# Performance work log

Hardware: AMD Instinct MI355X
Metric: run time of the kernel (lower is better)

Reference implementation:

```python
import jax, jax.numpy as jnp
import numpy as np

NUM_CLASSES = 80
AFS = 1024          # actors_features_size
OFS = 2048          # objects_features_size
NHEADS = 4
NHID = AFS // NHEADS + 4 // NHEADS   # 257
D = AFS + 4                           # 1028
ALPHA = 0.2                           # LeakyReLU slope
N_ACT, N_OBJ = 512, 3584


def _gat(x, adj_mask, W, a):
    # x: [N, D]; W: [H, D, NHID]; a: [H, 2*NHID]; adj_mask: [N, N] bool
    Wh = jnp.einsum('nf,hfd->hnd', x, W)                      # [H, N, NHID]
    f1 = jnp.einsum('hnd,hd->hn', Wh, a[:, :NHID])            # src score
    f2 = jnp.einsum('hnd,hd->hn', Wh, a[:, NHID:])            # dst score
    e = f1[:, :, None] + f2[:, None, :]                       # [H, N, N]
    e = jnp.where(e > 0, e, ALPHA * e)                        # LeakyReLU
    e = jnp.where(adj_mask[None], e, jnp.asarray(-9e15, e.dtype))
    att = jax.nn.softmax(e, axis=-1)                          # [H, N, N]
    h = jnp.einsum('hnm,hmd->hnd', att, Wh)                   # [H, N, NHID]
    h = jax.nn.elu(h)
    return jnp.transpose(h, (1, 0, 2)).reshape(x.shape[0], NHEADS * NHID)


def _ln(x, g, b):
    m = jnp.mean(x, axis=-1, keepdims=True)
    v = jnp.mean((x - m) ** 2, axis=-1, keepdims=True)
    return (x - m) * jax.lax.rsqrt(v + 1e-5) * g + b


def setup_inputs() -> dict:
    key = jax.random.key(0)
    ks = jax.random.split(key, 24)
    d = {
        'actors_features': jax.random.normal(ks[0], (N_ACT, 1024, 4, 7, 7), jnp.float32),
        'actors_labels': jax.random.uniform(ks[1], (N_ACT, NUM_CLASSES), jnp.float32),
        'actors_boxes': jax.random.uniform(ks[2], (N_ACT, 4), jnp.float32),
        'objects_features': jax.random.normal(ks[3], (N_OBJ, OFS), jnp.float32),
        'objects_boxes': jax.random.uniform(ks[4], (N_OBJ, 4), jnp.float32),
        'adj': jax.random.randint(ks[5], (N_ACT + N_OBJ, N_ACT + N_OBJ), 0, 2, jnp.int32),
    }
    s = lambda k, shp, fan: jax.random.normal(k, shp, jnp.float32) * (1.0 / np.sqrt(fan))
    d['obj_W'] = s(ks[6], (OFS, AFS), OFS)
    d['obj_b'] = jnp.zeros((AFS,), jnp.float32)
    d['gat1_W'] = s(ks[7], (NHEADS, D, NHID), D)
    d['gat1_a'] = s(ks[8], (NHEADS, 2 * NHID), 2 * NHID)
    d['gat_fc_W'] = s(ks[9], (D, D), D)
    d['gat_fc_b'] = jnp.zeros((D,), jnp.float32)
    d['ln1_g'] = jnp.ones((D,), jnp.float32)
    d['ln1_b'] = jnp.zeros((D,), jnp.float32)
    d['gat2_W'] = s(ks[10], (NHEADS, D, NHID), D)
    d['gat2_a'] = s(ks[11], (NHEADS, 2 * NHID), 2 * NHID)
    d['gat_fc2_W'] = s(ks[12], (D, D), D)
    d['gat_fc2_b'] = jnp.zeros((D,), jnp.float32)
    d['ln2_g'] = jnp.ones((D,), jnp.float32)
    d['ln2_b'] = jnp.zeros((D,), jnp.float32)
    d['logits_W'] = s(ks[13], (D, NUM_CLASSES), D)
    d['logits_b'] = jnp.zeros((NUM_CLASSES,), jnp.float32)
    return d


def reference(actors_features, actors_labels, actors_boxes, objects_features,
              objects_boxes, adj, obj_W, obj_b, gat1_W, gat1_a, gat_fc_W,
              gat_fc_b, ln1_g, ln1_b, gat2_W, gat2_a, gat_fc2_W, gat_fc2_b,
              ln2_g, ln2_b, logits_W, logits_b):
    ab, ob = actors_boxes, objects_boxes
    a_geo = jnp.stack([ab[:, 3] - ab[:, 1], ab[:, 2] - ab[:, 0],
                       (ab[:, 2] - ab[:, 0]) / 2 + ab[:, 0],
                       (ab[:, 3] - ab[:, 1]) / 2 + ab[:, 1]], axis=1)
    o_geo = jnp.stack([ob[:, 3] - ob[:, 1], ob[:, 2] - ob[:, 0],
                       (ob[:, 2] - ob[:, 0]) / 2 + ob[:, 0],
                       (ob[:, 3] - ob[:, 1]) / 2 + ob[:, 1]], axis=1)
    # torch.no_grad mean-pool over T,H,W -> [N, C]
    af = jax.lax.stop_gradient(jnp.mean(actors_features, axis=(2, 3, 4)))
    af = jnp.concatenate([af, a_geo], axis=1)                 # [Na, D]
    of = jax.nn.relu(objects_features @ obj_W + obj_b)        # reducer (OFS>AFS)
    of = jnp.concatenate([of, o_geo], axis=1)                 # [No, D]
    x = jnp.concatenate([af, of], axis=0)                     # [N, D]
    mask = adj > 0
    g = _gat(x, mask, gat1_W, gat1_a)
    x = _ln(x + g @ gat_fc_W + gat_fc_b, ln1_g, ln1_b)
    g = _gat(x, mask, gat2_W, gat2_a)
    x = _ln(x + g @ gat_fc2_W + gat_fc2_b, ln2_g, ln2_b)
    logits = x[:af.shape[0]] @ logits_W + logits_b            # [Na, C]
    y = actors_labels
    loss = jnp.mean(jnp.clip(logits, 0, None) - logits * y
                    + jnp.log1p(jnp.exp(-jnp.abs(logits))))
    return jax.nn.sigmoid(logits), loss
```

## Files before the change

### kernel.cpp

```cpp
#include <hip/hip_runtime.h>
#include <cstdint>

#define NACT 512
#define NOBJ 3584
#define NTOT 4096
#define DCOLS 1028
#define NHID_ 257
#define OFSZ 2048
#define KPAD 1056
#define NPADH 320
#define NPADFC 1088

typedef float f32x4 __attribute__((ext_vector_type(4)));
typedef short short8v __attribute__((ext_vector_type(8)));
typedef short short4v __attribute__((ext_vector_type(4)));

static const size_t OFF_X0    = 0;
static const size_t OFF_T     = 4210688;
static const size_t OFF_F1    = 8421376;
static const size_t OFF_F2    = 8437760;
static const size_t OFF_RMAX  = 8454144;
static const size_t OFF_RDEN  = 8470528;
static const size_t OFF_LOSSP = 8486912;
static const size_t OFF_MASK  = 8487424;
static const size_t OFF_XB    = 9011712;
static const size_t OFF_GB    = 11174400;
static const size_t OFF_OBJWT = 13337088;
static const size_t OFF_GATWT = 14385664;
static const size_t OFF_FCWT  = 15737344;
static const size_t OFF_WHT   = 16886272;

__device__ __forceinline__ short f2bf(float x) {
    unsigned u = __float_as_uint(x);
    u += 0x7fffu + ((u >> 16) & 1u);
    return (short)(u >> 16);
}
__device__ __forceinline__ int swz(int row, int chunk) {
    return row * 64 + (((chunk ^ ((row >> 1) & 3))) << 4);
}

__global__ void k_geo(const float* __restrict__ ab, const float* __restrict__ ob,
                      float* __restrict__ X) {
    int n = blockIdx.x * blockDim.x + threadIdx.x;
    if (n >= NTOT) return;
    const float* b = (n < NACT) ? &ab[n * 4] : &ob[(n - NACT) * 4];
    float x0 = b[0], y0 = b[1], x1 = b[2], y1 = b[3];
    float* o = &X[(size_t)n * DCOLS + 1024];
    o[0] = y1 - y0;
    o[1] = x1 - x0;
    o[2] = (x1 - x0) * 0.5f + x0;
    o[3] = (y1 - y0) * 0.5f + y0;
}

__global__ __launch_bounds__(256) void k_meanpool(const float* __restrict__ af,
                                                  float* __restrict__ X) {
    int w = blockIdx.x * 4 + (threadIdx.x >> 6);
    int lane = threadIdx.x & 63;
    const float* src = af + (size_t)w * 196;
    float s = src[lane] + src[lane + 64] + src[lane + 128];
    if (lane < 4) s += src[192 + lane];
    #pragma unroll
    for (int off = 32; off; off >>= 1) s += __shfl_down(s, off);
    if (lane == 0) {
        int n = w >> 10, c = w & 1023;
        X[(size_t)n * DCOLS + c] = s * (1.0f / 196.0f);
    }
}

__global__ __launch_bounds__(256) void k_packmask(const int* __restrict__ adj,
                                                  unsigned long long* __restrict__ mb) {
    int w = blockIdx.x * 4 + (threadIdx.x >> 6);
    int lane = threadIdx.x & 63;
    int v = adj[(size_t)w * 64 + lane];
    unsigned long long m = __ballot(v > 0);
    if (lane == 0) mb[w] = m;
}

__global__ __launch_bounds__(256) void k_transpW(const float* __restrict__ W, int K, int N,
                                                 short* __restrict__ Wt, int Kpad, int Npad) {
    __shared__ float Ws[32][33];
    int k0 = blockIdx.x * 32, n0 = blockIdx.y * 32;
    int t = threadIdx.x;
    #pragma unroll
    for (int i = 0; i < 4; ++i) {
        int j = t + i * 256;
        int r = j >> 5, c = j & 31;
        float v = 0.f;
        if (k0 + r < K && n0 + c < N) v = W[(size_t)(k0 + r) * N + n0 + c];
        Ws[r][c] = v;
    }
    __syncthreads();
    #pragma unroll
    for (int i = 0; i < 4; ++i) {
        int j = t + i * 256;
        int n = j >> 5, k = j & 31;
        Wt[(size_t)(n0 + n) * Kpad + k0 + k] = f2bf(Ws[k][n]);
    }
}

__global__ __launch_bounds__(256) void k_convX(const float* __restrict__ X,
                                               short* __restrict__ Xb) {
    int i = blockIdx.x * 256 + threadIdx.x;
    int n = i / 132, g = i % 132;
    int c0 = g * 8;
    short8v o;
    if (c0 + 8 <= DCOLS) {
        float4 v0 = *reinterpret_cast<const float4*>(&X[(size_t)n * DCOLS + c0]);
        float4 v1 = *reinterpret_cast<const float4*>(&X[(size_t)n * DCOLS + c0 + 4]);
        o[0]=f2bf(v0.x); o[1]=f2bf(v0.y); o[2]=f2bf(v0.z); o[3]=f2bf(v0.w);
        o[4]=f2bf(v1.x); o[5]=f2bf(v1.y); o[6]=f2bf(v1.z); o[7]=f2bf(v1.w);
    } else {
        #pragma unroll
        for (int j = 0; j < 8; ++j)
            o[j] = (c0 + j < DCOLS) ? f2bf(X[(size_t)n * DCOLS + c0 + j]) : (short)0;
    }
    *reinterpret_cast<short8v*>(&Xb[(size_t)n * KPAD + c0]) = o;
}

template <int MODE>
__global__ __launch_bounds__(256) void k_mm(
    const void* __restrict__ Aptr, int lda,
    const short* __restrict__ Bt, int ldb,
    void* __restrict__ Cptr, int ldc,
    const float* __restrict__ bias,
    const float* __restrict__ resid, int ldr,
    float* __restrict__ F1, float* __restrict__ F2,
    const float* __restrict__ RMAX, const float* __restrict__ RDEN,
    const unsigned long long* __restrict__ MB,
    const float* __restrict__ AV,
    int nk, int Nvalid) {
    __shared__ char sm[12288];
    const int t = threadIdx.x;
    const int m0 = blockIdx.x * 128;
    const int n0 = blockIdx.y * 64;
    const int z = blockIdx.z;

    short* Cwh = nullptr;
    short* Cgb = nullptr;
    float* Cf  = nullptr;
    int gcol = 0;
    if constexpr (MODE == 1) {
        Bt += (size_t)z * (NPADH * KPAD);
        Cwh = (short*)Cptr + (size_t)z * (NPADH * NTOT);
        AV += z * (2 * NHID_);
        F1 += z * NTOT; F2 += z * NTOT;
    } else if constexpr (MODE == 2) {
        Bt += (size_t)z * (NPADH * NTOT);
        F1 += z * NTOT; F2 += z * NTOT;
        RMAX += z * NTOT; RDEN += z * NTOT;
        Cgb = (short*)Cptr;
        gcol = z * NHID_;
    } else {
        Cf = (float*)Cptr;
    }

    const int ar = t >> 1, acp = t & 1;
    const int bn = t >> 2, bc = t & 3;
    float f1n = 0.f, rmx = 0.f, psc = 0.f;
    const unsigned long long* mrow = nullptr;
    const int pr = t & 127, pmh = t >> 7;
    if constexpr (MODE == 2) {
        int n = m0 + pr;
        f1n = F1[n];
        rmx = RMAX[n];
        psc = 1.0f / RDEN[n];
        mrow = MB + (size_t)n * 64;
    }

    const int wv = t >> 6, lane = t & 63, lr = lane & 15, lk = lane >> 4;
    const int aoff0 = swz(32 * wv + lr, lk);
    const int aoff1 = swz(32 * wv + 16 + lr, lk);
    int boff[4];
    #pragma unroll
    for (int cb = 0; cb < 4; ++cb) boff[cb] = 8192 + swz(16 * cb + lr, lk);

    f32x4 acc[2][4];
    #pragma unroll
    for (int i = 0; i < 2; ++i)
        #pragma unroll
        for (int j = 0; j < 4; ++j) acc[i][j] = (f32x4){0.f, 0.f, 0.f, 0.f};

    for (int kt = 0; kt < nk; ++kt) {
        const int k0 = kt * 32;
        if constexpr (MODE == 0) {
            const float* ap = (const float*)Aptr + (size_t)(m0 + ar) * lda + k0 + acp * 16;
            float4 u0 = *reinterpret_cast<const float4*>(ap);
            float4 u1 = *reinterpret_cast<const float4*>(ap + 4);
            float4 u2 = *reinterpret_cast<const float4*>(ap + 8);
            float4 u3 = *reinterpret_cast<const float4*>(ap + 12);
            short8v s0, s1;
            s0[0]=f2bf(u0.x); s0[1]=f2bf(u0.y); s0[2]=f2bf(u0.z); s0[3]=f2bf(u0.w);
            s0[4]=f2bf(u1.x); s0[5]=f2bf(u1.y); s0[6]=f2bf(u1.z); s0[7]=f2bf(u1.w);
            s1[0]=f2bf(u2.x); s1[1]=f2bf(u2.y); s1[2]=f2bf(u2.z); s1[3]=f2bf(u2.w);
            s1[4]=f2bf(u3.x); s1[5]=f2bf(u3.y); s1[6]=f2bf(u3.z); s1[7]=f2bf(u3.w);
            *reinterpret_cast<short8v*>(sm + swz(ar, 2 * acp)) = s0;
            *reinterpret_cast<short8v*>(sm + swz(ar, 2 * acp + 1)) = s1;
        } else if constexpr (MODE == 1 || MODE == 3) {
            const short* ap = (const short*)Aptr + (size_t)(m0 + ar) * lda + k0 + acp * 16;
            short8v v0 = *reinterpret_cast<const short8v*>(ap);
            short8v v1 = *reinterpret_cast<const short8v*>(ap + 8);
            *reinterpret_cast<short8v*>(sm + swz(ar, 2 * acp)) = v0;
            *reinterpret_cast<short8v*>(sm + swz(ar, 2 * acp + 1)) = v1;
        } else {
            const int mk = k0 + pmh * 16;
            unsigned long long w = mrow[mk >> 6];
            const int bb = mk & 63;
            const float* F2k = F2 + mk;
            float4 q0 = *reinterpret_cast<const float4*>(F2k);
            float4 q1 = *reinterpret_cast<const float4*>(F2k + 4);
            float4 q2 = *reinterpret_cast<const float4*>(F2k + 8);
            float4 q3 = *reinterpret_cast<const float4*>(F2k + 12);
            float fv[16] = {q0.x,q0.y,q0.z,q0.w, q1.x,q1.y,q1.z,q1.w,
                            q2.x,q2.y,q2.z,q2.w, q3.x,q3.y,q3.z,q3.w};
            short8v o0, o1;
            #pragma unroll
            for (int j = 0; j < 8; ++j) {
                float e = f1n + fv[j];
                e = e > 0.f ? e : 0.2f * e;
                float p = ((w >> (bb + j)) & 1ULL) ? __expf(e - rmx) * psc : 0.f;
                o0[j] = f2bf(p);
            }
            #pragma unroll
            for (int j = 0; j < 8; ++j) {
                float e = f1n + fv[8 + j];
                e = e > 0.f ? e : 0.2f * e;
                float p = ((w >> (bb + 8 + j)) & 1ULL) ? __expf(e - rmx) * psc : 0.f;
                o1[j] = f2bf(p);
            }
            *reinterpret_cast<short8v*>(sm + swz(pr, 2 * pmh)) = o0;
            *reinterpret_cast<short8v*>(sm + swz(pr, 2 * pmh + 1)) = o1;
        }
        {
            const short* bp = Bt + (size_t)(n0 + bn) * ldb + k0 + bc * 8;
            short8v v = *reinterpret_cast<const short8v*>(bp);
            *reinterpret_cast<short8v*>(sm + 8192 + swz(bn, bc)) = v;
        }
        __syncthreads();
        short8v a0 = *reinterpret_cast<short8v*>(sm + aoff0);
        short8v a1 = *reinterpret_cast<short8v*>(sm + aoff1);
        #pragma unroll
        for (int cb = 0; cb < 4; ++cb) {
            short8v b = *reinterpret_cast<short8v*>(sm + boff[cb]);
            acc[0][cb] = __builtin_amdgcn_mfma_f32_16x16x32_bf16(a0, b, acc[0][cb], 0, 0, 0);
            acc[1][cb] = __builtin_amdgcn_mfma_f32_16x16x32_bf16(a1, b, acc[1][cb], 0, 0, 0);
        }
        __syncthreads();
    }

    const int mb0 = m0 + 32 * wv + 4 * lk;
    if constexpr (MODE == 0 || MODE == 3) {
        #pragma unroll
        for (int rb = 0; rb < 2; ++rb)
            #pragma unroll
            for (int cb = 0; cb < 4; ++cb) {
                int c = n0 + 16 * cb + lr;
                if (c < Nvalid) {
                    #pragma unroll
                    for (int rr = 0; rr < 4; ++rr) {
                        int m = mb0 + 16 * rb + rr;
                        float v = acc[rb][cb][rr] + bias[c];
                        if constexpr (MODE == 0) v = fmaxf(v, 0.f);
                        if constexpr (MODE == 3) v += resid[(size_t)m * ldr + c];
                        Cf[(size_t)m * ldc + c] = v;
                    }
                }
            }
    } else if constexpr (MODE == 1) {
        float la1[4], la2[4];
        #pragma unroll
        for (int cb = 0; cb < 4; ++cb) {
            int d = n0 + 16 * cb + lr;
            la1[cb] = (d < NHID_) ? AV[d] : 0.f;
            la2[cb] = (d < NHID_) ? AV[NHID_ + d] : 0.f;
        }
        #pragma unroll
        for (int rb = 0; rb < 2; ++rb) {
            #pragma unroll
            for (int cb = 0; cb < 4; ++cb) {
                int d = n0 + 16 * cb + lr;
                short4v o;
                o[0] = f2bf(acc[rb][cb][0]); o[1] = f2bf(acc[rb][cb][1]);
                o[2] = f2bf(acc[rb][cb][2]); o[3] = f2bf(acc[rb][cb][3]);
                *reinterpret_cast<short4v*>(&Cwh[(size_t)d * NTOT + mb0 + 16 * rb]) = o;
            }
            #pragma unroll
            for (int rr = 0; rr < 4; ++rr) {
                float s1 = 0.f, s2 = 0.f;
                #pragma unroll
                for (int cb = 0; cb < 4; ++cb) {
                    s1 += acc[rb][cb][rr] * la1[cb];
                    s2 += acc[rb][cb][rr] * la2[cb];
                }
                #pragma unroll
                for (int mk = 1; mk < 16; mk <<= 1) {
                    s1 += __shfl_xor(s1, mk);
                    s2 += __shfl_xor(s2, mk);
                }
                if (lr == 0) {
                    int m = mb0 + 16 * rb + rr;
                    atomicAdd(&F1[m], s1);
                    atomicAdd(&F2[m], s2);
                }
            }
        }
    } else {
        #pragma unroll
        for (int rb = 0; rb < 2; ++rb)
            #pragma unroll
            for (int cb = 0; cb < 4; ++cb) {
                int d = n0 + 16 * cb + lr;
                if (d < NHID_) {
                    #pragma unroll
                    for (int rr = 0; rr < 4; ++rr) {
                        int m = mb0 + 16 * rb + rr;
                        float v = acc[rb][cb][rr];
                        v = v > 0.f ? v : expm1f(v);
                        Cgb[(size_t)m * KPAD + gcol + d] = f2bf(v);
                    }
                }
            }
    }
}

__global__ __launch_bounds__(256) void k_rowstat(const float* __restrict__ F1,
                                                 const float* __restrict__ F2,
                                                 const unsigned long long* __restrict__ mb,
                                                 float* __restrict__ RMAX, float* __restrict__ RDEN) {
    __shared__ float f2s[NTOT];
    __shared__ unsigned long long mw[4][64];
    int h = blockIdx.y;
    const float4* src = reinterpret_cast<const float4*>(F2 + (size_t)h * NTOT);
    float4* dst = reinterpret_cast<float4*>(f2s);
    for (int i = threadIdx.x; i < NTOT / 4; i += 256) dst[i] = src[i];
    int wv = threadIdx.x >> 6, lane = threadIdx.x & 63;
    int n = blockIdx.x * 4 + wv;
    mw[wv][lane] = mb[(size_t)n * 64 + lane];
    __syncthreads();
    float f1n = F1[(size_t)h * NTOT + n];
    float rm = -1e30f, rs = 0.f;
    for (int b = 0; b < 64; ++b) {
        unsigned long long wb = mw[wv][b];
        if ((wb >> lane) & 1ULL) {
            float e = f1n + f2s[b * 64 + lane];
            e = e > 0.f ? e : 0.2f * e;
            if (e > rm) { rs *= __expf(rm - e); rm = e; }
            rs += __expf(e - rm);
        }
    }
    #pragma unroll
    for (int off = 32; off; off >>= 1) {
        float m2 = __shfl_down(rm, off), s2 = __shfl_down(rs, off);
        float nm = fmaxf(rm, m2);
        rs = rs * __expf(rm - nm) + s2 * __expf(m2 - nm);
        rm = nm;
    }
    if (lane == 0) {
        if (rs == 0.f) rs = 1.f;
        RMAX[(size_t)h * NTOT + n] = rm;
        RDEN[(size_t)h * NTOT + n] = rs;
    }
}

__global__ __launch_bounds__(256) void k_ln(const float* __restrict__ T,
                                            const float* __restrict__ g,
                                            const float* __restrict__ b,
                                            float* __restrict__ O) {
    int n = blockIdx.x;
    const float* row = T + (size_t)n * DCOLS;
    float s = 0.f, q = 0.f;
    for (int i = threadIdx.x; i < DCOLS / 4; i += 256) {
        float4 v = *reinterpret_cast<const float4*>(&row[i * 4]);
        s += v.x + v.y + v.z + v.w;
        q += v.x * v.x + v.y * v.y + v.z * v.z + v.w * v.w;
    }
    __shared__ float ls[2][4];
    int lane = threadIdx.x & 63, wv = threadIdx.x >> 6;
    #pragma unroll
    for (int off = 32; off; off >>= 1) {
        s += __shfl_down(s, off);
        q += __shfl_down(q, off);
    }
    if (lane == 0) { ls[0][wv] = s; ls[1][wv] = q; }
    __syncthreads();
    s = ls[0][0] + ls[0][1] + ls[0][2] + ls[0][3];
    q = ls[1][0] + ls[1][1] + ls[1][2] + ls[1][3];
    float mean = s * (1.0f / DCOLS);
    float var = q * (1.0f / DCOLS) - mean * mean;
    float rstd = rsqrtf(var + 1e-5f);
    float* orow = O + (size_t)n * DCOLS;
    for (int i = threadIdx.x; i < DCOLS; i += 256)
        orow[i] = (row[i] - mean) * rstd * g[i] + b[i];
}

__global__ __launch_bounds__(128) void k_logits(const float* __restrict__ X,
                                                const float* __restrict__ W,
                                                const float* __restrict__ bias,
                                                const float* __restrict__ Y,
                                                float* __restrict__ out,
                                                float* __restrict__ lossp) {
    __shared__ float xs[DCOLS];
    int n = blockIdx.x;
    for (int i = threadIdx.x; i < DCOLS / 4; i += 128)
        *reinterpret_cast<float4*>(&xs[i * 4]) =
            *reinterpret_cast<const float4*>(&X[(size_t)n * DCOLS + i * 4]);
    __syncthreads();
    float loss = 0.f;
    int c = threadIdx.x;
    if (c < 80) {
        float acc = bias[c];
        for (int k = 0; k < DCOLS; ++k) acc += xs[k] * W[k * 80 + c];
        out[n * 80 + c] = 1.0f / (1.0f + expf(-acc));
        float y = Y[n * 80 + c];
        loss = fmaxf(acc, 0.f) - acc * y + log1pf(expf(-fabsf(acc)));
    }
    __shared__ float lr[2];
    int lane = threadIdx.x & 63, wv = threadIdx.x >> 6;
    #pragma unroll
    for (int off = 32; off; off >>= 1) loss += __shfl_down(loss, off);
    if (lane == 0) lr[wv] = loss;
    __syncthreads();
    if (threadIdx.x == 0) lossp[n] = lr[0] + lr[1];
}

__global__ __launch_bounds__(256) void k_lossfin(const float* __restrict__ lossp,
                                                 float* __restrict__ out) {
    float s = 0.f;
    for (int i = threadIdx.x; i < NACT; i += 256) s += lossp[i];
    #pragma unroll
    for (int off = 32; off; off >>= 1) s += __shfl_down(s, off);
    __shared__ float lr[4];
    int lane = threadIdx.x & 63, wv = threadIdx.x >> 6;
    if (lane == 0) lr[wv] = s;
    __syncthreads();
    if (threadIdx.x == 0) out[NACT * 80] = (lr[0] + lr[1] + lr[2] + lr[3]) / (float)(NACT * 80);
}

extern "C" void kernel_launch(void* const* d_in, const int* in_sizes, int n_in,
                              void* d_out, int out_size, void* d_ws, size_t ws_size,
                              hipStream_t stream) {
    const float* actors_features  = (const float*)d_in[0];
    const float* actors_labels    = (const float*)d_in[1];
    const float* actors_boxes     = (const float*)d_in[2];
    const float* objects_features = (const float*)d_in[3];
    const float* objects_boxes    = (const float*)d_in[4];
    const int*   adj              = (const int*)d_in[5];
    const float* obj_W    = (const float*)d_in[6];
    const float* obj_b    = (const float*)d_in[7];
    const float* gatW[2]  = {(const float*)d_in[8],  (const float*)d_in[14]};
    const float* gatA[2]  = {(const float*)d_in[9],  (const float*)d_in[15]};
    const float* fcW[2]   = {(const float*)d_in[10], (const float*)d_in[16]};
    const float* fcB[2]   = {(const float*)d_in[11], (const float*)d_in[17]};
    const float* lnG[2]   = {(const float*)d_in[12], (const float*)d_in[18]};
    const float* lnB[2]   = {(const float*)d_in[13], (const float*)d_in[19]};
    const float* logits_W = (const float*)d_in[20];
    const float* logits_b = (const float*)d_in[21];
    float* out = (float*)d_out;

    float* ws   = (float*)d_ws;
    float* X0   = ws + OFF_X0;
    float* T    = ws + OFF_T;
    float* F1   = ws + OFF_F1;
    float* F2   = ws + OFF_F2;
    float* RMAX = ws + OFF_RMAX;
    float* RDEN = ws + OFF_RDEN;
    float* LOSSP= ws + OFF_LOSSP;
    unsigned long long* MASK = (unsigned long long*)(ws + OFF_MASK);
    short* Xb    = (short*)(ws + OFF_XB);
    short* Gb    = (short*)(ws + OFF_GB);
    short* objWt = (short*)(ws + OFF_OBJWT);
    short* gatWt = (short*)(ws + OFF_GATWT);
    short* fcWt  = (short*)(ws + OFF_FCWT);
    short* WHT   = (short*)(ws + OFF_WHT);

    hipMemsetAsync(F1, 0, 2 * 4 * NTOT * sizeof(float), stream);
    hipMemsetAsync(Gb, 0, (size_t)NTOT * KPAD * 2, stream);

    k_geo<<<(NTOT + 255) / 256, 256, 0, stream>>>(actors_boxes, objects_boxes, X0);
    k_meanpool<<<(NACT * 1024) / 4, 256, 0, stream>>>(actors_features, X0);
    k_packmask<<<(NTOT * 64) / 4, 256, 0, stream>>>(adj, MASK);

    k_transpW<<<dim3(64, 32), 256, 0, stream>>>(obj_W, OFSZ, 1024, objWt, OFSZ, 1024);
    for (int L = 0; L < 2; ++L) {
        for (int h = 0; h < 4; ++h)
            k_transpW<<<dim3(33, 10), 256, 0, stream>>>(
                gatW[L] + (size_t)h * DCOLS * NHID_, DCOLS, NHID_,
                gatWt + (size_t)(L * 4 + h) * NPADH * KPAD, KPAD, NPADH);
        k_transpW<<<dim3(33, 34), 256, 0, stream>>>(
            fcW[L], DCOLS, DCOLS, fcWt + (size_t)L * NPADFC * KPAD, KPAD, NPADFC);
    }

    k_mm<0><<<dim3(NOBJ / 128, 16, 1), 256, 0, stream>>>(
        objects_features, OFSZ, objWt, OFSZ, X0 + (size_t)NACT * DCOLS, DCOLS,
        obj_b, nullptr, 0, nullptr, nullptr, nullptr, nullptr, nullptr, nullptr,
        OFSZ / 32, 1024);

    k_convX<<<(NTOT * 132) / 256, 256, 0, stream>>>(X0, Xb);

    const float* xin = X0;
    for (int L = 0; L < 2; ++L) {
        if (L == 1)
            hipMemsetAsync(F1, 0, 2 * 4 * NTOT * sizeof(float), stream);
        if (L == 1)
            k_convX<<<(NTOT * 132) / 256, 256, 0, stream>>>(T, Xb);
        k_mm<1><<<dim3(NTOT / 128, NPADH / 64, 4), 256, 0, stream>>>(
            Xb, KPAD, gatWt + (size_t)L * 4 * NPADH * KPAD, KPAD, WHT, 0,
            nullptr, nullptr, 0, F1, F2, nullptr, nullptr, nullptr, gatA[L],
            KPAD / 32, NHID_);
        k_rowstat<<<dim3(NTOT / 4, 4), 256, 0, stream>>>(F1, F2, MASK, RMAX, RDEN);
        k_mm<2><<<dim3(NTOT / 128, NPADH / 64, 4), 256, 0, stream>>>(
            nullptr, 0, WHT, NTOT, Gb, 0,
            nullptr, nullptr, 0, F1, F2, RMAX, RDEN, MASK, nullptr,
            NTOT / 32, NHID_);
        k_mm<3><<<dim3(NTOT / 128, NPADFC / 64, 1), 256, 0, stream>>>(
            Gb, KPAD, fcWt + (size_t)L * NPADFC * KPAD, KPAD, T, DCOLS,
            fcB[L], xin, DCOLS, nullptr, nullptr, nullptr, nullptr, nullptr, nullptr,
            KPAD / 32, DCOLS);
        k_ln<<<NTOT, 256, 0, stream>>>(T, lnG[L], lnB[L], T);
        xin = T;
    }
    k_logits<<<NACT, 128, 0, stream>>>(T, logits_W, logits_b, actors_labels, out, LOSSP);
    k_lossfin<<<1, 256, 0, stream>>>(LOSSP, out);
}
```

Baseline: 1.599 ms.

## Enlarge GEMM tiles to 128x128 and split attention-PV into dedicated full-width kernel

The generic bf16 MFMA GEMM moves from 128x64 to 128x128 tiles with a 2x2 wave layout and 16 accumulators per wave, raising arithmetic intensity. Output padding grows to 384 and 1152 columns to match. The attention-times-values stage moves into a new kernel, k_pv, where each block covers 64 rows against all 384 padded hidden columns of a head. Each probability tile is then computed once instead of once per 64-column slice, cutting redundant exp and mask work and repeated F2 reads. The cost is more padded compute, higher register pressure, and fewer blocks per launch (256 for k_pv), which may underfill the GPU.

```diff
diff --git a/kernel.cpp b/kernel.cpp
--- a/kernel.cpp
+++ b/kernel.cpp
@@ -8,8 +8,8 @@
 #define NHID_ 257
 #define OFSZ 2048
 #define KPAD 1056
-#define NPADH 320
-#define NPADFC 1088
+#define NPADH 384
+#define NPADFC 1152
 
 typedef float f32x4 __attribute__((ext_vector_type(4)));
 typedef short short8v __attribute__((ext_vector_type(8)));
@@ -27,8 +27,8 @@
 static const size_t OFF_GB    = 11174400;
 static const size_t OFF_OBJWT = 13337088;
 static const size_t OFF_GATWT = 14385664;
-static const size_t OFF_FCWT  = 15737344;
-static const size_t OFF_WHT   = 16886272;
+static const size_t OFF_FCWT  = 16007680;
+static const size_t OFF_WHT   = 17224192;
 
 __device__ __forceinline__ short f2bf(float x) {
     unsigned u = __float_as_uint(x);
@@ -118,65 +118,44 @@
 }
 
 template <int MODE>
-__global__ __launch_bounds__(256) void k_mm(
+__global__ __launch_bounds__(256, 2) void k_mm(
     const void* __restrict__ Aptr, int lda,
     const short* __restrict__ Bt, int ldb,
     void* __restrict__ Cptr, int ldc,
     const float* __restrict__ bias,
     const float* __restrict__ resid, int ldr,
     float* __restrict__ F1, float* __restrict__ F2,
-    const float* __restrict__ RMAX, const float* __restrict__ RDEN,
-    const unsigned long long* __restrict__ MB,
     const float* __restrict__ AV,
     int nk, int Nvalid) {
-    __shared__ char sm[12288];
+    __shared__ char sm[16384];
     const int t = threadIdx.x;
     const int m0 = blockIdx.x * 128;
-    const int n0 = blockIdx.y * 64;
+    const int n0 = blockIdx.y * 128;
     const int z = blockIdx.z;
 
     short* Cwh = nullptr;
-    short* Cgb = nullptr;
     float* Cf  = nullptr;
-    int gcol = 0;
     if constexpr (MODE == 1) {
         Bt += (size_t)z * (NPADH * KPAD);
-        Cwh = (short*)Cptr + (size_t)z * (NPADH * NTOT);
+        Cwh = (short*)Cptr + (size_t)z * ((size_t)NPADH * NTOT);
         AV += z * (2 * NHID_);
         F1 += z * NTOT; F2 += z * NTOT;
-    } else if constexpr (MODE == 2) {
-        Bt += (size_t)z * (NPADH * NTOT);
-        F1 += z * NTOT; F2 += z * NTOT;
-        RMAX += z * NTOT; RDEN += z * NTOT;
-        Cgb = (short*)Cptr;
-        gcol = z * NHID_;
     } else {
         Cf = (float*)Cptr;
     }
 
     const int ar = t >> 1, acp = t & 1;
-    const int bn = t >> 2, bc = t & 3;
-    float f1n = 0.f, rmx = 0.f, psc = 0.f;
-    const unsigned long long* mrow = nullptr;
-    const int pr = t & 127, pmh = t >> 7;
-    if constexpr (MODE == 2) {
-        int n = m0 + pr;
-        f1n = F1[n];
-        rmx = RMAX[n];
-        psc = 1.0f / RDEN[n];
-        mrow = MB + (size_t)n * 64;
-    }
-
     const int wv = t >> 6, lane = t & 63, lr = lane & 15, lk = lane >> 4;
-    const int aoff0 = swz(32 * wv + lr, lk);
-    const int aoff1 = swz(32 * wv + 16 + lr, lk);
-    int boff[4];
-    #pragma unroll
-    for (int cb = 0; cb < 4; ++cb) boff[cb] = 8192 + swz(16 * cb + lr, lk);
-
-    f32x4 acc[2][4];
-    #pragma unroll
-    for (int i = 0; i < 2; ++i)
+    const int wr = wv >> 1, wc = wv & 1;
+    int aoff[4], boff[4];
+    #pragma unroll
+    for (int i = 0; i < 4; ++i) aoff[i] = swz(64 * wr + 16 * i + lr, lk);
+    #pragma unroll
+    for (int j = 0; j < 4; ++j) boff[j] = 8192 + swz(64 * wc + 16 * j + lr, lk);
+
+    f32x4 acc[4][4];
+    #pragma unroll
+    for (int i = 0; i < 4; ++i)
         #pragma unroll
         for (int j = 0; j < 4; ++j) acc[i][j] = (f32x4){0.f, 0.f, 0.f, 0.f};
 
@@ -195,101 +174,78 @@
             s1[4]=f2bf(u3.x); s1[5]=f2bf(u3.y); s1[6]=f2bf(u3.z); s1[7]=f2bf(u3.w);
             *reinterpret_cast<short8v*>(sm + swz(ar, 2 * acp)) = s0;
             *reinterpret_cast<short8v*>(sm + swz(ar, 2 * acp + 1)) = s1;
-        } else if constexpr (MODE == 1 || MODE == 3) {
+        } else {
             const short* ap = (const short*)Aptr + (size_t)(m0 + ar) * lda + k0 + acp * 16;
             short8v v0 = *reinterpret_cast<const short8v*>(ap);
             short8v v1 = *reinterpret_cast<const short8v*>(ap + 8);
             *reinterpret_cast<short8v*>(sm + swz(ar, 2 * acp)) = v0;
             *reinterpret_cast<short8v*>(sm + swz(ar, 2 * acp + 1)) = v1;
-        } else {
-            const int mk = k0 + pmh * 16;
-            unsigned long long w = mrow[mk >> 6];
-            const int bb = mk & 63;
-            const float* F2k = F2 + mk;
-            float4 q0 = *reinterpret_cast<const float4*>(F2k);
-            float4 q1 = *reinterpret_cast<const float4*>(F2k + 4);
-            float4 q2 = *reinterpret_cast<const float4*>(F2k + 8);
-            float4 q3 = *reinterpret_cast<const float4*>(F2k + 12);
-            float fv[16] = {q0.x,q0.y,q0.z,q0.w, q1.x,q1.y,q1.z,q1.w,
-                            q2.x,q2.y,q2.z,q2.w, q3.x,q3.y,q3.z,q3.w};
-            short8v o0, o1;
-            #pragma unroll
-            for (int j = 0; j < 8; ++j) {
-                float e = f1n + fv[j];
-                e = e > 0.f ? e : 0.2f * e;
-                float p = ((w >> (bb + j)) & 1ULL) ? __expf(e - rmx) * psc : 0.f;
-                o0[j] = f2bf(p);
-            }
-            #pragma unroll
-            for (int j = 0; j < 8; ++j) {
-                float e = f1n + fv[8 + j];
-                e = e > 0.f ? e : 0.2f * e;
-                float p = ((w >> (bb + 8 + j)) & 1ULL) ? __expf(e - rmx) * psc : 0.f;
-                o1[j] = f2bf(p);
-            }
-            *reinterpret_cast<short8v*>(sm + swz(pr, 2 * pmh)) = o0;
-            *reinterpret_cast<short8v*>(sm + swz(pr, 2 * pmh + 1)) = o1;
         }
         {
-            const short* bp = Bt + (size_t)(n0 + bn) * ldb + k0 + bc * 8;
-            short8v v = *reinterpret_cast<const short8v*>(bp);
-            *reinterpret_cast<short8v*>(sm + 8192 + swz(bn, bc)) = v;
+            const short* bp = Bt + (size_t)(n0 + ar) * ldb + k0 + acp * 16;
+            short8v v0 = *reinterpret_cast<const short8v*>(bp);
+            short8v v1 = *reinterpret_cast<const short8v*>(bp + 8);
+            *reinterpret_cast<short8v*>(sm + 8192 + swz(ar, 2 * acp)) = v0;
+            *reinterpret_cast<short8v*>(sm + 8192 + swz(ar, 2 * acp + 1)) = v1;
         }
         __syncthreads();
-        short8v a0 = *reinterpret_cast<short8v*>(sm + aoff0);
-        short8v a1 = *reinterpret_cast<short8v*>(sm + aoff1);
-        #pragma unroll
-        for (int cb = 0; cb < 4; ++cb) {
-            short8v b = *reinterpret_cast<short8v*>(sm + boff[cb]);
-            acc[0][cb] = __builtin_amdgcn_mfma_f32_16x16x32_bf16(a0, b, acc[0][cb], 0, 0, 0);
-            acc[1][cb] = __builtin_amdgcn_mfma_f32_16x16x32_bf16(a1, b, acc[1][cb], 0, 0, 0);
-        }
+        short8v a[4], b[4];
+        #pragma unroll
+        for (int i = 0; i < 4; ++i) a[i] = *reinterpret_cast<short8v*>(sm + aoff[i]);
+        #pragma unroll
+        for (int j = 0; j < 4; ++j) b[j] = *reinterpret_cast<short8v*>(sm + boff[j]);
+        #pragma unroll
+        for (int i = 0; i < 4; ++i)
+            #pragma unroll
+            for (int j = 0; j < 4; ++j)
+                acc[i][j] = __builtin_amdgcn_mfma_f32_16x16x32_bf16(a[i], b[j], acc[i][j], 0, 0, 0);
         __syncthreads();
     }
 
-    const int mb0 = m0 + 32 * wv + 4 * lk;
+    const int mb0 = m0 + 64 * wr + 4 * lk;
+    const int cb0 = n0 + 64 * wc + lr;
     if constexpr (MODE == 0 || MODE == 3) {
         #pragma unroll
-        for (int rb = 0; rb < 2; ++rb)
-            #pragma unroll
-            for (int cb = 0; cb < 4; ++cb) {
-                int c = n0 + 16 * cb + lr;
+        for (int i = 0; i < 4; ++i)
+            #pragma unroll
+            for (int j = 0; j < 4; ++j) {
+                int c = cb0 + 16 * j;
                 if (c < Nvalid) {
                     #pragma unroll
                     for (int rr = 0; rr < 4; ++rr) {
-                        int m = mb0 + 16 * rb + rr;
-                        float v = acc[rb][cb][rr] + bias[c];
+                        int m = mb0 + 16 * i + rr;
+                        float v = acc[i][j][rr] + bias[c];
                         if constexpr (MODE == 0) v = fmaxf(v, 0.f);
                         if constexpr (MODE == 3) v += resid[(size_t)m * ldr + c];
                         Cf[(size_t)m * ldc + c] = v;
                     }
                 }
             }
-    } else if constexpr (MODE == 1) {
+    } else {
         float la1[4], la2[4];
         #pragma unroll
-        for (int cb = 0; cb < 4; ++cb) {
-            int d = n0 + 16 * cb + lr;
-            la1[cb] = (d < NHID_) ? AV[d] : 0.f;
-            la2[cb] = (d < NHID_) ? AV[NHID_ + d] : 0.f;
-        }
-        #pragma unroll
-        for (int rb = 0; rb < 2; ++rb) {
-            #pragma unroll
-            for (int cb = 0; cb < 4; ++cb) {
-                int d = n0 + 16 * cb + lr;
+        for (int j = 0; j < 4; ++j) {
+            int d = cb0 + 16 * j;
+            la1[j] = (d < NHID_) ? AV[d] : 0.f;
+            la2[j] = (d < NHID_) ? AV[NHID_ + d] : 0.f;
+        }
+        #pragma unroll
+        for (int i = 0; i < 4; ++i) {
+            #pragma unroll
+            for (int j = 0; j < 4; ++j) {
+                int d = cb0 + 16 * j;
                 short4v o;
-                o[0] = f2bf(acc[rb][cb][0]); o[1] = f2bf(acc[rb][cb][1]);
-                o[2] = f2bf(acc[rb][cb][2]); o[3] = f2bf(acc[rb][cb][3]);
-                *reinterpret_cast<short4v*>(&Cwh[(size_t)d * NTOT + mb0 + 16 * rb]) = o;
+                o[0] = f2bf(acc[i][j][0]); o[1] = f2bf(acc[i][j][1]);
+                o[2] = f2bf(acc[i][j][2]); o[3] = f2bf(acc[i][j][3]);
+                *reinterpret_cast<short4v*>(&Cwh[(size_t)d * NTOT + mb0 + 16 * i]) = o;
             }
             #pragma unroll
             for (int rr = 0; rr < 4; ++rr) {
                 float s1 = 0.f, s2 = 0.f;
                 #pragma unroll
-                for (int cb = 0; cb < 4; ++cb) {
-                    s1 += acc[rb][cb][rr] * la1[cb];
-                    s2 += acc[rb][cb][rr] * la2[cb];
+                for (int j = 0; j < 4; ++j) {
+                    s1 += acc[i][j][rr] * la1[j];
+                    s2 += acc[i][j][rr] * la2[j];
                 }
                 #pragma unroll
                 for (int mk = 1; mk < 16; mk <<= 1) {
@@ -297,28 +253,107 @@
                     s2 += __shfl_xor(s2, mk);
                 }
                 if (lr == 0) {
-                    int m = mb0 + 16 * rb + rr;
+                    int m = mb0 + 16 * i + rr;
                     atomicAdd(&F1[m], s1);
                     atomicAdd(&F2[m], s2);
                 }
             }
         }
-    } else {
-        #pragma unroll
-        for (int rb = 0; rb < 2; ++rb)
-            #pragma unroll
-            for (int cb = 0; cb < 4; ++cb) {
-                int d = n0 + 16 * cb + lr;
-                if (d < NHID_) {
-                    #pragma unroll
-                    for (int rr = 0; rr < 4; ++rr) {
-                        int m = mb0 + 16 * rb + rr;
-                        float v = acc[rb][cb][rr];
-                        v = v > 0.f ? v : expm1f(v);
-                        Cgb[(size_t)m * KPAD + gcol + d] = f2bf(v);
-                    }
+    }
+}
+
+__global__ __launch_bounds__(256, 1) void k_pv(
+    const short* __restrict__ WHT,
+    const float* __restrict__ F1, const float* __restrict__ F2,
+    const float* __restrict__ RMAX, const float* __restrict__ RDEN,
+    const unsigned long long* __restrict__ MB,
+    short* __restrict__ Gb) {
+    __shared__ char sm[28672];
+    const int t = threadIdx.x;
+    const int m0 = blockIdx.x * 64;
+    const int h = blockIdx.z;
+    const short* WhH = WHT + (size_t)h * ((size_t)NPADH * NTOT);
+    const float* F1h = F1 + h * NTOT;
+    const float* F2h = F2 + h * NTOT;
+    const int gcol = h * NHID_;
+
+    const int pr = t >> 2, pq = t & 3;
+    const int n = m0 + pr;
+    const float f1n = F1h[n];
+    const float rmx = RMAX[h * NTOT + n];
+    const float psc = 1.0f / RDEN[h * NTOT + n];
+    const unsigned long long* mrow = MB + (size_t)n * 64;
+
+    const int vr = t >> 1, vcp = t & 1;
+
+    const int wv = t >> 6, lane = t & 63, lr = lane & 15, lk = lane >> 4;
+    int aoff[4], boff[6];
+    #pragma unroll
+    for (int i = 0; i < 4; ++i) aoff[i] = swz(16 * i + lr, lk);
+    #pragma unroll
+    for (int j = 0; j < 6; ++j) boff[j] = 4096 + swz(96 * wv + 16 * j + lr, lk);
+
+    f32x4 acc[4][6];
+    #pragma unroll
+    for (int i = 0; i < 4; ++i)
+        #pragma unroll
+        for (int j = 0; j < 6; ++j) acc[i][j] = (f32x4){0.f, 0.f, 0.f, 0.f};
+
+    for (int kt = 0; kt < NTOT / 32; ++kt) {
+        const int k0 = kt * 32;
+        {
+            const int mk = k0 + pq * 8;
+            unsigned long long wbits = mrow[k0 >> 6] >> ((k0 & 63) + pq * 8);
+            float4 q0 = *reinterpret_cast<const float4*>(F2h + mk);
+            float4 q1 = *reinterpret_cast<const float4*>(F2h + mk + 4);
+            float fv[8] = {q0.x, q0.y, q0.z, q0.w, q1.x, q1.y, q1.z, q1.w};
+            short8v o;
+            #pragma unroll
+            for (int j = 0; j < 8; ++j) {
+                float e = f1n + fv[j];
+                e = e > 0.f ? e : 0.2f * e;
+                float p = ((wbits >> j) & 1ULL) ? __expf(e - rmx) * psc : 0.f;
+                o[j] = f2bf(p);
+            }
+            *reinterpret_cast<short8v*>(sm + swz(pr, pq)) = o;
+        }
+        #pragma unroll
+        for (int rep = 0; rep < 3; ++rep) {
+            int row = vr + rep * 128;
+            const short* vp = WhH + (size_t)row * NTOT + k0 + vcp * 16;
+            short8v v0 = *reinterpret_cast<const short8v*>(vp);
+            short8v v1 = *reinterpret_cast<const short8v*>(vp + 8);
+            *reinterpret_cast<short8v*>(sm + 4096 + swz(row, 2 * vcp)) = v0;
+            *reinterpret_cast<short8v*>(sm + 4096 + swz(row, 2 * vcp + 1)) = v1;
+        }
+        __syncthreads();
+        short8v a[4], b[6];
+        #pragma unroll
+        for (int i = 0; i < 4; ++i) a[i] = *reinterpret_cast<short8v*>(sm + aoff[i]);
+        #pragma unroll
+        for (int j = 0; j < 6; ++j) b[j] = *reinterpret_cast<short8v*>(sm + boff[j]);
+        #pragma unroll
+        for (int i = 0; i < 4; ++i)
+            #pragma unroll
+            for (int j = 0; j < 6; ++j)
+                acc[i][j] = __builtin_amdgcn_mfma_f32_16x16x32_bf16(a[i], b[j], acc[i][j], 0, 0, 0);
+        __syncthreads();
+    }
+
+    #pragma unroll
+    for (int j = 0; j < 6; ++j) {
+        int d = 96 * wv + 16 * j + lr;
+        if (d < NHID_) {
+            #pragma unroll
+            for (int i = 0; i < 4; ++i)
+                #pragma unroll
+                for (int rr = 0; rr < 4; ++rr) {
+                    int m = m0 + 16 * i + 4 * lk + rr;
+                    float v = acc[i][j][rr];
+                    v = v > 0.f ? v : expm1f(v);
+                    Gb[(size_t)m * KPAD + gcol + d] = f2bf(v);
                 }
-            }
+        }
     }
 }
 
@@ -482,38 +517,36 @@
     k_transpW<<<dim3(64, 32), 256, 0, stream>>>(obj_W, OFSZ, 1024, objWt, OFSZ, 1024);
     for (int L = 0; L < 2; ++L) {
         for (int h = 0; h < 4; ++h)
-            k_transpW<<<dim3(33, 10), 256, 0, stream>>>(
+            k_transpW<<<dim3(33, 12), 256, 0, stream>>>(
                 gatW[L] + (size_t)h * DCOLS * NHID_, DCOLS, NHID_,
                 gatWt + (size_t)(L * 4 + h) * NPADH * KPAD, KPAD, NPADH);
-        k_transpW<<<dim3(33, 34), 256, 0, stream>>>(
+        k_transpW<<<dim3(33, 36), 256, 0, stream>>>(
             fcW[L], DCOLS, DCOLS, fcWt + (size_t)L * NPADFC * KPAD, KPAD, NPADFC);
     }
 
-    k_mm<0><<<dim3(NOBJ / 128, 16, 1), 256, 0, stream>>>(
+    k_mm<0><<<dim3(NOBJ / 128, 1024 / 128, 1), 256, 0, stream>>>(
         objects_features, OFSZ, objWt, OFSZ, X0 + (size_t)NACT * DCOLS, DCOLS,
-        obj_b, nullptr, 0, nullptr, nullptr, nullptr, nullptr, nullptr, nullptr,
+        obj_b, nullptr, 0, nullptr, nullptr, nullptr,
         OFSZ / 32, 1024);
 
     k_convX<<<(NTOT * 132) / 256, 256, 0, stream>>>(X0, Xb);
 
     const float* xin = X0;
     for (int L = 0; L < 2; ++L) {
-        if (L == 1)
+        if (L == 1) {
             hipMemsetAsync(F1, 0, 2 * 4 * NTOT * sizeof(float), stream);
-        if (L == 1)
             k_convX<<<(NTOT * 132) / 256, 256, 0, stream>>>(T, Xb);
-        k_mm<1><<<dim3(NTOT / 128, NPADH / 64, 4), 256, 0, stream>>>(
+        }
+        k_mm<1><<<dim3(NTOT / 128, NPADH / 128, 4), 256, 0, stream>>>(
             Xb, KPAD, gatWt + (size_t)L * 4 * NPADH * KPAD, KPAD, WHT, 0,
-            nullptr, nullptr, 0, F1, F2, nullptr, nullptr, nullptr, gatA[L],
+            nullptr, nullptr, 0, F1, F2, gatA[L],
             KPAD / 32, NHID_);
         k_rowstat<<<dim3(NTOT / 4, 4), 256, 0, stream>>>(F1, F2, MASK, RMAX, RDEN);
-        k_mm<2><<<dim3(NTOT / 128, NPADH / 64, 4), 256, 0, stream>>>(
-            nullptr, 0, WHT, NTOT, Gb, 0,
-            nullptr, nullptr, 0, F1, F2, RMAX, RDEN, MASK, nullptr,
-            NTOT / 32, NHID_);
-        k_mm<3><<<dim3(NTOT / 128, NPADFC / 64, 1), 256, 0, stream>>>(
+        k_pv<<<dim3(NTOT / 64, 1, 4), 256, 0, stream>>>(
+            WHT, F1, F2, RMAX, RDEN, MASK, Gb);
+        k_mm<3><<<dim3(NTOT / 128, NPADFC / 128, 1), 256, 0, stream>>>(
             Gb, KPAD, fcWt + (size_t)L * NPADFC * KPAD, KPAD, T, DCOLS,
-            fcB[L], xin, DCOLS, nullptr, nullptr, nullptr, nullptr, nullptr, nullptr,
+            fcB[L], xin, DCOLS, nullptr, nullptr, nullptr,
             KPAD / 32, DCOLS);
         k_ln<<<NTOT, 256, 0, stream>>>(T, lnG[L], lnB[L], T);
         xin = T;
```

Result: faster. 1.558 ms (-2.6%).
